# Optimization experiments

Measured on AMD Instinct MI355X. Metric: run time of the kernel, lower is better.

The kernel has to match this reference:

```python
import jax, jax.numpy as jnp
import numpy as np

B, N, M = 32, 512, 32          # batch frames, atoms, neighbors
H_A = 64                        # atom embedding dim
DMIN, DMAX, STEP = 0.0, 10.0, 0.1
FILTERS = jnp.arange(DMIN, DMAX + STEP, STEP, dtype=jnp.float32)  # [101]
H_B = FILTERS.shape[0]
N_CONV = 4
N_CLASSES = 10
BN_EPS = 1e-5


def setup_inputs() -> dict:
    key = jax.random.key(0)
    ks = jax.random.split(key, 6)
    return {
        "nbr_adj_dist": jax.random.uniform(ks[0], (B, N, M), jnp.float32) * DMAX,
        "nbr_adj_list": jax.random.randint(ks[1], (B, N, M), 0, N),
        "emb_w": jax.random.normal(ks[2], (N, H_A), jnp.float32),
        "fc_w": jax.random.normal(ks[3], (N_CONV, 2 * H_A + H_B, 2 * H_A), jnp.float32) * 0.05,
        "fc_b": jnp.zeros((N_CONV, 2 * H_A), jnp.float32),
        "bn1_g": jnp.ones((N_CONV, 2 * H_A), jnp.float32),
        "bn1_b": jnp.zeros((N_CONV, 2 * H_A), jnp.float32),
        "bn2_g": jnp.ones((N_CONV, H_A), jnp.float32),
        "bn2_b": jnp.zeros((N_CONV, H_A), jnp.float32),
        "cls_w": jax.random.normal(ks[4], (H_A, N_CLASSES), jnp.float32) * 0.05,
        "cls_b": jnp.zeros((N_CLASSES,), jnp.float32),
    }


def _bn(x2d, g, b):
    # training-mode BatchNorm1d over flattened batch axis (biased variance)
    mu = x2d.mean(axis=0)
    var = x2d.var(axis=0)
    return g * (x2d - mu) * jax.lax.rsqrt(var + BN_EPS) + b


def reference(nbr_adj_dist, nbr_adj_list, emb_w, fc_w, fc_b,
              bn1_g, bn1_b, bn2_g, bn2_b, cls_w, cls_b):
    # 1. Gaussian basis expansion of neighbor distances: [B,N,M,H_B]
    nbr_emb = jnp.exp(-((nbr_adj_dist[..., None] - FILTERS) ** 2) / (STEP ** 2))
    # 2. atom embeddings: atom_emb_idx = arange(N) per batch element
    atom = jnp.broadcast_to(emb_w[None], (B, N, H_A))
    # 3. CGCNN-style graph convolutions
    for l in range(N_CONV):
        # neighbor gather per batch: [B,N,M,H_A]
        nbrs = jax.vmap(lambda e, idx: e[idx])(atom, nbr_adj_list)
        total = jnp.concatenate(
            [jnp.broadcast_to(atom[:, :, None, :], (B, N, M, H_A)), nbrs, nbr_emb],
            axis=-1)                                        # [B,N,M,2*H_A+H_B]
        gated = jnp.einsum('bnmf,fh->bnmh', total, fc_w[l]) + fc_b[l]
        gated = _bn(gated.reshape(-1, 2 * H_A), bn1_g[l], bn1_b[l]).reshape(B, N, M, 2 * H_A)
        filt, core = jnp.split(gated, 2, axis=-1)
        summed = jnp.sum(jax.nn.sigmoid(filt) * jax.nn.relu(core), axis=2)  # [B,N,H_A]
        summed = _bn(summed.reshape(-1, H_A), bn2_g[l], bn2_b[l]).reshape(B, N, H_A)
        atom = jax.nn.relu(atom + summed)  # layer-internal residual
    # 4-6. activation, mean pooling over atoms, classifier, softmax
    emb = jax.nn.relu(atom)
    pooled = jnp.sum(emb, axis=1) / N                      # [B,H_A]
    logits = pooled @ cls_w + cls_b                        # [B,n_classes]
    return jax.nn.softmax(logits, axis=-1)
```

## Files before the change

kernel.cpp:

```cpp
#include <hip/hip_runtime.h>
#include <math.h>

constexpr int kB   = 32;
constexpr int kN   = 512;
constexpr int kM   = 32;
constexpr int kHA  = 64;
constexpr int kHB  = 101;
constexpr int kHO  = 128;
constexpr int kNF  = 229;
constexpr int kRows = kB * kN;
constexpr long kTRows = (long)kRows * kM;
constexpr int kNCls = 10;
constexpr float kEps = 1e-5f;
constexpr int kG    = 16;
constexpr int kNB   = kRows / kG;
constexpr int kT    = 512;
constexpr int kTaps = 8;

__global__ void k_init_atom(const float* __restrict__ emb, float* __restrict__ atom) {
    int i = blockIdx.x * blockDim.x + threadIdx.x;
    atom[i] = emb[i & (kN * kHA - 1)];
}

template<bool RESID>
__global__ __launch_bounds__(256)
void k_pre(const float* __restrict__ atomIn, float* __restrict__ atomOut,
           const float* __restrict__ summed, const float* __restrict__ sc2,
           const float* __restrict__ W, const float* __restrict__ bias,
           float* __restrict__ preA, float* __restrict__ preB) {
    __shared__ float sA[32 * 64];
    int t = threadIdx.x;
    int r0 = blockIdx.x * 32;
    for (int i = t; i < 32 * 64; i += 256) {
        int r = i >> 6, h = i & 63;
        float v = atomIn[(r0 + r) * 64 + h];
        if (RESID) {
            float x = fmaf(summed[(r0 + r) * 64 + h], sc2[h], sc2[64 + h]);
            v = fmaxf(v + x, 0.f);
            atomOut[(r0 + r) * 64 + h] = v;
        }
        sA[i] = v;
    }
    __syncthreads();
    int cg = t & 31, rg = t >> 5;
    const float* Wb = W + cg * 4;
    float4 accA[4], accB[4];
    float4 b4 = *(const float4*)&bias[cg * 4];
    #pragma unroll
    for (int r = 0; r < 4; ++r) {
        accA[r] = b4;
        accB[r] = make_float4(0.f, 0.f, 0.f, 0.f);
    }
    for (int k = 0; k < 64; ++k) {
        float4 wA = *(const float4*)&Wb[k * kHO];
        float4 wB = *(const float4*)&Wb[(64 + k) * kHO];
        #pragma unroll
        for (int r = 0; r < 4; ++r) {
            float a = sA[(rg * 4 + r) * 64 + k];
            accA[r].x = fmaf(a, wA.x, accA[r].x);
            accA[r].y = fmaf(a, wA.y, accA[r].y);
            accA[r].z = fmaf(a, wA.z, accA[r].z);
            accA[r].w = fmaf(a, wA.w, accA[r].w);
            accB[r].x = fmaf(a, wB.x, accB[r].x);
            accB[r].y = fmaf(a, wB.y, accB[r].y);
            accB[r].z = fmaf(a, wB.z, accB[r].z);
            accB[r].w = fmaf(a, wB.w, accB[r].w);
        }
    }
    #pragma unroll
    for (int r = 0; r < 4; ++r) {
        int row = r0 + rg * 4 + r;
        *(float4*)&preA[row * kHO + cg * 4] = accA[r];
        *(float4*)&preB[row * kHO + cg * 4] = accB[r];
    }
}

__device__ __forceinline__ void setup_tiles(int t, int blk,
        const float* __restrict__ dist, const int* __restrict__ nbrs,
        float (*wv)[kM][kTaps], int (*roff)[kM], int (*wbase)[kM]) {
    int g = t >> 5, m = t & 31;
    int p = blk * kG + g;
    float d = dist[p * kM + m];
    int kc = (int)floorf(d * 10.f);
    int ks = min(max(kc - 3, 0), kHB - kTaps);
    wbase[g][m] = ks * kHO;
    roff[g][m] = (((p >> 9) << 9) + nbrs[p * kM + m]) * kHO;
    #pragma unroll
    for (int j = 0; j < kTaps; ++j) {
        float dd = d - 0.1f * (float)(ks + j);
        wv[g][m][j] = __expf(-100.f * dd * dd);
    }
}

__device__ __forceinline__ void compute_x(const float* __restrict__ W3s,
        const float* __restrict__ wvp, int wb, int ro, int cg,
        const float* __restrict__ preB, float2 pa01, float2 pa23,
        float& x0, float& x1, float& x2, float& x3) {
    float2 xb01 = *(const float2*)&preB[ro + 2 * cg];
    float2 xb23 = *(const float2*)&preB[ro + 64 + 2 * cg];
    x0 = pa01.x + xb01.x; x1 = pa01.y + xb01.y;
    x2 = pa23.x + xb23.x; x3 = pa23.y + xb23.y;
    float warr[kTaps];
    *(float4*)&warr[0] = *(const float4*)&wvp[0];
    *(float4*)&warr[4] = *(const float4*)&wvp[4];
    const float* base = &W3s[wb + 2 * cg];
    #pragma unroll
    for (int j = 0; j < kTaps; ++j) {
        float2 a = *(const float2*)&base[j * kHO];
        float2 b = *(const float2*)&base[j * kHO + 64];
        x0 = fmaf(warr[j], a.x, x0);
        x1 = fmaf(warr[j], a.y, x1);
        x2 = fmaf(warr[j], b.x, x2);
        x3 = fmaf(warr[j], b.y, x3);
    }
}

__global__ __launch_bounds__(kT, 4)
void k_stats(const float* __restrict__ dist, const int* __restrict__ nbrs,
             const float* __restrict__ preA, const float* __restrict__ preB,
             const float* __restrict__ W3, float* __restrict__ part1) {
    __shared__ float W3s[kHB * kHO];
    __shared__ float wv[kG][kM][kTaps];
    __shared__ int   roff[kG][kM];
    __shared__ int   wbase[kG][kM];
    __shared__ float red[1024];
    int t = threadIdx.x;
    for (int i = t; i < kHB * kHO; i += kT) W3s[i] = W3[i];
    setup_tiles(t, blockIdx.x, dist, nbrs, wv, roff, wbase);
    __syncthreads();
    int cg = t & 31, ms = t >> 5;
    float S[4] = {0.f, 0.f, 0.f, 0.f}, SS[4] = {0.f, 0.f, 0.f, 0.f};
    for (int g = 0; g < kG; ++g) {
        int p = blockIdx.x * kG + g;
        float2 pa01 = *(const float2*)&preA[p * kHO + 2 * cg];
        float2 pa23 = *(const float2*)&preA[p * kHO + 64 + 2 * cg];
        #pragma unroll
        for (int mm = 0; mm < 2; ++mm) {
            int m = ms + mm * 16;
            float x0, x1, x2, x3;
            compute_x(W3s, &wv[g][m][0], wbase[g][m], roff[g][m], cg,
                      preB, pa01, pa23, x0, x1, x2, x3);
            S[0] += x0; S[1] += x1; S[2] += x2; S[3] += x3;
            SS[0] = fmaf(x0, x0, SS[0]); SS[1] = fmaf(x1, x1, SS[1]);
            SS[2] = fmaf(x2, x2, SS[2]); SS[3] = fmaf(x3, x3, SS[3]);
        }
    }
    #pragma unroll
    for (int c = 0; c < 4; ++c) {
        S[c]  += __shfl_xor(S[c], 32);
        SS[c] += __shfl_xor(SS[c], 32);
    }
    int w = t >> 6;
    if ((t & 63) < 32)
        *(float4*)&red[(w * 32 + cg) * 4] = make_float4(S[0], S[1], S[2], S[3]);
    __syncthreads();
    if (t < 128) {
        int c = t >> 5, cc = t & 31;
        float s = 0.f;
        #pragma unroll
        for (int ww = 0; ww < 8; ++ww) s += red[(ww * 32 + cc) * 4 + c];
        int ch = (c < 2) ? (2 * cc + c) : (64 + 2 * cc + (c - 2));
        part1[blockIdx.x * 256 + ch] = s;
    }
    __syncthreads();
    if ((t & 63) < 32)
        *(float4*)&red[(w * 32 + cg) * 4] = make_float4(SS[0], SS[1], SS[2], SS[3]);
    __syncthreads();
    if (t < 128) {
        int c = t >> 5, cc = t & 31;
        float s = 0.f;
        #pragma unroll
        for (int ww = 0; ww < 8; ++ww) s += red[(ww * 32 + cc) * 4 + c];
        int ch = (c < 2) ? (2 * cc + c) : (64 + 2 * cc + (c - 2));
        part1[blockIdx.x * 256 + 128 + ch] = s;
    }
}

__global__ __launch_bounds__(256)
void k_bn1r(const float* __restrict__ part1, const float* __restrict__ g,
            const float* __restrict__ bb, float* __restrict__ sc) {
    __shared__ float red[256];
    int t = threadIdx.x;
    float a0 = 0.f, a1 = 0.f, a2 = 0.f, a3 = 0.f;
    for (int r = 0; r < kNB; r += 4) {
        a0 += part1[(r + 0) * 256 + t];
        a1 += part1[(r + 1) * 256 + t];
        a2 += part1[(r + 2) * 256 + t];
        a3 += part1[(r + 3) * 256 + t];
    }
    red[t] = (a0 + a1) + (a2 + a3);
    __syncthreads();
    if (t < 128) {
        float inv = 1.f / (float)kTRows;
        float mu = red[t] * inv;
        float var = red[128 + t] * inv - mu * mu;
        float scale = g[t] * rsqrtf(var + kEps);
        sc[t] = scale;
        sc[128 + t] = bb[t] - mu * scale;
    }
}

__global__ __launch_bounds__(kT, 4)
void k_apply(const float* __restrict__ dist, const int* __restrict__ nbrs,
             const float* __restrict__ preA, const float* __restrict__ preB,
             const float* __restrict__ W3, const float* __restrict__ sc,
             float* __restrict__ summed, float* __restrict__ part2) {
    __shared__ float W3s[kHB * kHO];
    __shared__ float wv[kG][kM][kTaps];
    __shared__ int   roff[kG][kM];
    __shared__ int   wbase[kG][kM];
    __shared__ float red[1024];
    int t = threadIdx.x;
    for (int i = t; i < kHB * kHO; i += kT) W3s[i] = W3[i];
    setup_tiles(t, blockIdx.x, dist, nbrs, wv, roff, wbase);
    int cg = t & 31, ms = t >> 5;
    float scf0 = sc[2 * cg],       scf1 = sc[2 * cg + 1];
    float shf0 = sc[128 + 2 * cg], shf1 = sc[128 + 2 * cg + 1];
    float scc0 = sc[64 + 2 * cg],  scc1 = sc[64 + 2 * cg + 1];
    float shc0 = sc[192 + 2 * cg], shc1 = sc[192 + 2 * cg + 1];
    __syncthreads();
    float S2 = 0.f, SS2 = 0.f;
    for (int g = 0; g < kG; ++g) {
        int p = blockIdx.x * kG + g;
        float2 pa01 = *(const float2*)&preA[p * kHO + 2 * cg];
        float2 pa23 = *(const float2*)&preA[p * kHO + 64 + 2 * cg];
        float s0 = 0.f, s1 = 0.f;
        #pragma unroll
        for (int mm = 0; mm < 2; ++mm) {
            int m = ms + mm * 16;
            float x0, x1, x2, x3;
            compute_x(W3s, &wv[g][m][0], wbase[g][m], roff[g][m], cg,
                      preB, pa01, pa23, x0, x1, x2, x3);
            float yf0 = fmaf(x0, scf0, shf0);
            float yf1 = fmaf(x1, scf1, shf1);
            float yc0 = fmaf(x2, scc0, shc0);
            float yc1 = fmaf(x3, scc1, shc1);
            float sg0 = 1.f / (1.f + __expf(-yf0));
            float sg1 = 1.f / (1.f + __expf(-yf1));
            s0 = fmaf(sg0, fmaxf(yc0, 0.f), s0);
            s1 = fmaf(sg1, fmaxf(yc1, 0.f), s1);
        }
        *(float2*)&red[(ms * 32 + cg) * 2] = make_float2(s0, s1);
        __syncthreads();
        if (t < 64) {
            float v = 0.f;
            #pragma unroll
            for (int m2 = 0; m2 < 16; ++m2)
                v += red[(m2 * 32 + (t >> 1)) * 2 + (t & 1)];
            summed[p * kHA + t] = v;
            S2 += v;
            SS2 = fmaf(v, v, SS2);
        }
        __syncthreads();
    }
    if (t < 64) {
        part2[blockIdx.x * kHO + t] = S2;
        part2[blockIdx.x * kHO + 64 + t] = SS2;
    }
}

__global__ __launch_bounds__(128)
void k_bn2r(const float* __restrict__ part2, const float* __restrict__ g,
            const float* __restrict__ bb, float* __restrict__ sc) {
    __shared__ float red[128];
    int t = threadIdx.x;
    float a0 = 0.f, a1 = 0.f, a2 = 0.f, a3 = 0.f;
    for (int r = 0; r < kNB; r += 4) {
        a0 += part2[(r + 0) * kHO + t];
        a1 += part2[(r + 1) * kHO + t];
        a2 += part2[(r + 2) * kHO + t];
        a3 += part2[(r + 3) * kHO + t];
    }
    red[t] = (a0 + a1) + (a2 + a3);
    __syncthreads();
    if (t < 64) {
        float inv = 1.f / (float)kRows;
        float mu = red[t] * inv;
        float var = red[64 + t] * inv - mu * mu;
        float scale = g[t] * rsqrtf(var + kEps);
        sc[t] = scale;
        sc[64 + t] = bb[t] - mu * scale;
    }
}

__global__ __launch_bounds__(1024)
void k_final(const float* __restrict__ atom, const float* __restrict__ summed,
             const float* __restrict__ sc2, const float* __restrict__ cw,
             const float* __restrict__ cb, float* __restrict__ out) {
    __shared__ float red[1024];
    __shared__ float pooled[kHA];
    __shared__ float lg[kNCls];
    int b = blockIdx.x, t = threadIdx.x;
    int h = t & 63, q = t >> 6;
    const float* ab = atom + (long)b * kN * kHA;
    const float* sb = summed + (long)b * kN * kHA;
    float scv = sc2[h], shv = sc2[64 + h];
    float s = 0.f;
    for (int n = q * 32; n < q * 32 + 32; ++n) {
        float v = ab[n * 64 + h] + fmaf(sb[n * 64 + h], scv, shv);
        s += fmaxf(v, 0.f);
    }
    red[t] = s;
    __syncthreads();
    if (t < 64) {
        float v = 0.f;
        #pragma unroll
        for (int qq = 0; qq < 16; ++qq) v += red[qq * 64 + t];
        pooled[t] = v * (1.f / kN);
    }
    __syncthreads();
    if (t < kNCls) {
        float acc = cb[t];
        #pragma unroll
        for (int k = 0; k < kHA; ++k) acc = fmaf(pooled[k], cw[k * kNCls + t], acc);
        lg[t] = acc;
    }
    __syncthreads();
    if (t == 0) {
        float mx = lg[0];
        for (int c = 1; c < kNCls; ++c) mx = fmaxf(mx, lg[c]);
        float e[kNCls], se = 0.f;
        for (int c = 0; c < kNCls; ++c) { e[c] = __expf(lg[c] - mx); se += e[c]; }
        float inv = 1.f / se;
        for (int c = 0; c < kNCls; ++c) out[b * kNCls + c] = e[c] * inv;
    }
}

extern "C" void kernel_launch(void* const* d_in, const int* in_sizes, int n_in,
                              void* d_out, int out_size, void* d_ws, size_t ws_size,
                              hipStream_t stream) {
    const float* dist = (const float*)d_in[0];
    const int*   nbrs = (const int*)d_in[1];
    const float* emb  = (const float*)d_in[2];
    const float* fcw  = (const float*)d_in[3];
    const float* fcb  = (const float*)d_in[4];
    const float* bn1g = (const float*)d_in[5];
    const float* bn1b = (const float*)d_in[6];
    const float* bn2g = (const float*)d_in[7];
    const float* bn2b = (const float*)d_in[8];
    const float* clw  = (const float*)d_in[9];
    const float* clb  = (const float*)d_in[10];
    float* out = (float*)d_out;

    float* ws     = (float*)d_ws;
    float* atom   = ws;
    float* preA   = atom + kRows * kHA;
    float* preB   = preA + kRows * kHO;
    float* summed = preB + kRows * kHO;
    float* part1  = summed + kRows * kHA;
    float* part2  = part1 + kNB * 256;
    float* bn1sc  = part2 + kNB * kHO;
    float* bn2sc  = bn1sc + 256;

    k_init_atom<<<dim3(kRows * kHA / 256), dim3(256), 0, stream>>>(emb, atom);
    for (int l = 0; l < 4; ++l) {
        const float* W  = fcw + (long)l * kNF * kHO;
        const float* W3 = W + 2 * kHA * kHO;
        if (l == 0)
            k_pre<false><<<dim3(kRows / 32), dim3(256), 0, stream>>>(
                atom, atom, nullptr, nullptr, W, fcb + l * kHO, preA, preB);
        else
            k_pre<true><<<dim3(kRows / 32), dim3(256), 0, stream>>>(
                atom, atom, summed, bn2sc, W, fcb + l * kHO, preA, preB);
        k_stats<<<dim3(kNB), dim3(kT), 0, stream>>>(dist, nbrs, preA, preB, W3, part1);
        k_bn1r<<<dim3(1), dim3(256), 0, stream>>>(part1, bn1g + l * kHO, bn1b + l * kHO, bn1sc);
        k_apply<<<dim3(kNB), dim3(kT), 0, stream>>>(dist, nbrs, preA, preB, W3, bn1sc,
                                                    summed, part2);
        k_bn2r<<<dim3(1), dim3(128), 0, stream>>>(part2, bn2g + l * kHA, bn2b + l * kHA, bn2sc);
    }
    k_final<<<dim3(kB), dim3(1024), 0, stream>>>(atom, summed, bn2sc, clw, clb, out);
}
```

Before: 810.7 us.

## Fuse BN reductions via atomics, store W3 as fp16, interleave channels, halve group size

```diff
diff --git a/kernel.cpp b/kernel.cpp
--- a/kernel.cpp
+++ b/kernel.cpp
@@ -1,5 +1,8 @@
 #include <hip/hip_runtime.h>
 #include <math.h>
+
+typedef _Float16 half_t;
+typedef __attribute__((ext_vector_type(4))) _Float16 half4;
 
 constexpr int kB   = 32;
 constexpr int kN   = 512;
@@ -12,11 +15,15 @@
 constexpr long kTRows = (long)kRows * kM;
 constexpr int kNCls = 10;
 constexpr float kEps = 1e-5f;
-constexpr int kG    = 16;
+constexpr int kG    = 8;
 constexpr int kNB   = kRows / kG;
 constexpr int kT    = 512;
 constexpr int kTaps = 8;
 
+__device__ __forceinline__ int origCh(int j) {
+    return ((j & 1) << 6) + ((j >> 2) << 1) + ((j >> 1) & 1);
+}
+
 __global__ void k_init_atom(const float* __restrict__ emb, float* __restrict__ atom) {
     int i = blockIdx.x * blockDim.x + threadIdx.x;
     atom[i] = emb[i & (kN * kHA - 1)];
@@ -25,121 +32,128 @@
 template<bool RESID>
 __global__ __launch_bounds__(256)
 void k_pre(const float* __restrict__ atomIn, float* __restrict__ atomOut,
-           const float* __restrict__ summed, const float* __restrict__ sc2,
+           const float* __restrict__ summed, const float* __restrict__ acc2,
+           const float* __restrict__ g2, const float* __restrict__ b2,
            const float* __restrict__ W, const float* __restrict__ bias,
-           float* __restrict__ preA, float* __restrict__ preB) {
+           float* __restrict__ preA, float* __restrict__ preB,
+           float* __restrict__ bn1acc, float* __restrict__ zeroBuf) {
     __shared__ float sA[32 * 64];
+    __shared__ float sc2s[128];
     int t = threadIdx.x;
+    if (blockIdx.x == 0) {
+        bn1acc[t] = 0.f;
+        if (t < 128) zeroBuf[t] = 0.f;
+    }
+    if (RESID) {
+        if (t < 64) {
+            float inv = 1.f / (float)kRows;
+            float mu = acc2[t] * inv;
+            float var = acc2[64 + t] * inv - mu * mu;
+            float sc = g2[t] * rsqrtf(var + kEps);
+            sc2s[t] = sc;
+            sc2s[64 + t] = b2[t] - mu * sc;
+        }
+        __syncthreads();
+    }
     int r0 = blockIdx.x * 32;
     for (int i = t; i < 32 * 64; i += 256) {
-        int r = i >> 6, h = i & 63;
-        float v = atomIn[(r0 + r) * 64 + h];
+        float v = atomIn[r0 * 64 + i];
         if (RESID) {
-            float x = fmaf(summed[(r0 + r) * 64 + h], sc2[h], sc2[64 + h]);
-            v = fmaxf(v + x, 0.f);
-            atomOut[(r0 + r) * 64 + h] = v;
+            int h = i & 63;
+            v = fmaxf(v + fmaf(summed[r0 * 64 + i], sc2s[h], sc2s[64 + h]), 0.f);
+            atomOut[r0 * 64 + i] = v;
         }
         sA[i] = v;
     }
     __syncthreads();
     int cg = t & 31, rg = t >> 5;
-    const float* Wb = W + cg * 4;
+    float2 bb01 = *(const float2*)&bias[2 * cg];
+    float2 bb23 = *(const float2*)&bias[64 + 2 * cg];
     float4 accA[4], accB[4];
-    float4 b4 = *(const float4*)&bias[cg * 4];
     #pragma unroll
     for (int r = 0; r < 4; ++r) {
-        accA[r] = b4;
+        accA[r] = make_float4(bb01.x, bb23.x, bb01.y, bb23.y);
         accB[r] = make_float4(0.f, 0.f, 0.f, 0.f);
     }
     for (int k = 0; k < 64; ++k) {
-        float4 wA = *(const float4*)&Wb[k * kHO];
-        float4 wB = *(const float4*)&Wb[(64 + k) * kHO];
+        float2 wA01 = *(const float2*)&W[k * kHO + 2 * cg];
+        float2 wA23 = *(const float2*)&W[k * kHO + 64 + 2 * cg];
+        float2 wB01 = *(const float2*)&W[(64 + k) * kHO + 2 * cg];
+        float2 wB23 = *(const float2*)&W[(64 + k) * kHO + 64 + 2 * cg];
         #pragma unroll
         for (int r = 0; r < 4; ++r) {
             float a = sA[(rg * 4 + r) * 64 + k];
-            accA[r].x = fmaf(a, wA.x, accA[r].x);
-            accA[r].y = fmaf(a, wA.y, accA[r].y);
-            accA[r].z = fmaf(a, wA.z, accA[r].z);
-            accA[r].w = fmaf(a, wA.w, accA[r].w);
-            accB[r].x = fmaf(a, wB.x, accB[r].x);
-            accB[r].y = fmaf(a, wB.y, accB[r].y);
-            accB[r].z = fmaf(a, wB.z, accB[r].z);
-            accB[r].w = fmaf(a, wB.w, accB[r].w);
+            accA[r].x = fmaf(a, wA01.x, accA[r].x);
+            accA[r].y = fmaf(a, wA23.x, accA[r].y);
+            accA[r].z = fmaf(a, wA01.y, accA[r].z);
+            accA[r].w = fmaf(a, wA23.y, accA[r].w);
+            accB[r].x = fmaf(a, wB01.x, accB[r].x);
+            accB[r].y = fmaf(a, wB23.x, accB[r].y);
+            accB[r].z = fmaf(a, wB01.y, accB[r].z);
+            accB[r].w = fmaf(a, wB23.y, accB[r].w);
         }
     }
     #pragma unroll
     for (int r = 0; r < 4; ++r) {
         int row = r0 + rg * 4 + r;
-        *(float4*)&preA[row * kHO + cg * 4] = accA[r];
-        *(float4*)&preB[row * kHO + cg * 4] = accB[r];
-    }
-}
-
-__device__ __forceinline__ void setup_tiles(int t, int blk,
-        const float* __restrict__ dist, const int* __restrict__ nbrs,
-        float (*wv)[kM][kTaps], int (*roff)[kM], int (*wbase)[kM]) {
-    int g = t >> 5, m = t & 31;
-    int p = blk * kG + g;
-    float d = dist[p * kM + m];
-    int kc = (int)floorf(d * 10.f);
-    int ks = min(max(kc - 3, 0), kHB - kTaps);
-    wbase[g][m] = ks * kHO;
-    roff[g][m] = (((p >> 9) << 9) + nbrs[p * kM + m]) * kHO;
-    #pragma unroll
-    for (int j = 0; j < kTaps; ++j) {
-        float dd = d - 0.1f * (float)(ks + j);
-        wv[g][m][j] = __expf(-100.f * dd * dd);
-    }
-}
-
-__device__ __forceinline__ void compute_x(const float* __restrict__ W3s,
-        const float* __restrict__ wvp, int wb, int ro, int cg,
-        const float* __restrict__ preB, float2 pa01, float2 pa23,
-        float& x0, float& x1, float& x2, float& x3) {
-    float2 xb01 = *(const float2*)&preB[ro + 2 * cg];
-    float2 xb23 = *(const float2*)&preB[ro + 64 + 2 * cg];
-    x0 = pa01.x + xb01.x; x1 = pa01.y + xb01.y;
-    x2 = pa23.x + xb23.x; x3 = pa23.y + xb23.y;
-    float warr[kTaps];
-    *(float4*)&warr[0] = *(const float4*)&wvp[0];
-    *(float4*)&warr[4] = *(const float4*)&wvp[4];
-    const float* base = &W3s[wb + 2 * cg];
-    #pragma unroll
-    for (int j = 0; j < kTaps; ++j) {
-        float2 a = *(const float2*)&base[j * kHO];
-        float2 b = *(const float2*)&base[j * kHO + 64];
-        x0 = fmaf(warr[j], a.x, x0);
-        x1 = fmaf(warr[j], a.y, x1);
-        x2 = fmaf(warr[j], b.x, x2);
-        x3 = fmaf(warr[j], b.y, x3);
-    }
-}
-
-__global__ __launch_bounds__(kT, 4)
+        *(float4*)&preA[row * kHO + 4 * cg] = accA[r];
+        *(float4*)&preB[row * kHO + 4 * cg] = accB[r];
+    }
+}
+
+__global__ __launch_bounds__(kT, 6)
 void k_stats(const float* __restrict__ dist, const int* __restrict__ nbrs,
              const float* __restrict__ preA, const float* __restrict__ preB,
-             const float* __restrict__ W3, float* __restrict__ part1) {
-    __shared__ float W3s[kHB * kHO];
+             const float* __restrict__ W3, float* __restrict__ acc) {
+    __shared__ half_t W3h[kHB * kHO];
     __shared__ float wv[kG][kM][kTaps];
     __shared__ int   roff[kG][kM];
     __shared__ int   wbase[kG][kM];
-    __shared__ float red[1024];
+    __shared__ float red[2048];
     int t = threadIdx.x;
-    for (int i = t; i < kHB * kHO; i += kT) W3s[i] = W3[i];
-    setup_tiles(t, blockIdx.x, dist, nbrs, wv, roff, wbase);
+    int lb = (int)(blockIdx.x & 7) * (kNB / 8) + (int)(blockIdx.x >> 3);
+    for (int i = t; i < kHB * kHO; i += kT)
+        W3h[i] = (half_t)W3[(i & ~127) + origCh(i & 127)];
+    if (t < kG * kM) {
+        int g = t >> 5, m = t & 31;
+        int p = lb * kG + g;
+        float d = dist[p * kM + m];
+        int kc = (int)floorf(d * 10.f);
+        int ks = min(max(kc - 3, 0), kHB - kTaps);
+        wbase[g][m] = ks * kHO;
+        roff[g][m] = (((p >> 9) << 9) + nbrs[p * kM + m]) * kHO;
+        #pragma unroll
+        for (int j = 0; j < kTaps; ++j) {
+            float dd = d - 0.1f * (float)(ks + j);
+            wv[g][m][j] = __expf(-100.f * dd * dd);
+        }
+    }
     __syncthreads();
     int cg = t & 31, ms = t >> 5;
     float S[4] = {0.f, 0.f, 0.f, 0.f}, SS[4] = {0.f, 0.f, 0.f, 0.f};
     for (int g = 0; g < kG; ++g) {
-        int p = blockIdx.x * kG + g;
-        float2 pa01 = *(const float2*)&preA[p * kHO + 2 * cg];
-        float2 pa23 = *(const float2*)&preA[p * kHO + 64 + 2 * cg];
+        int p = lb * kG + g;
+        float4 pa = *(const float4*)&preA[p * kHO + 4 * cg];
         #pragma unroll
         for (int mm = 0; mm < 2; ++mm) {
             int m = ms + mm * 16;
-            float x0, x1, x2, x3;
-            compute_x(W3s, &wv[g][m][0], wbase[g][m], roff[g][m], cg,
-                      preB, pa01, pa23, x0, x1, x2, x3);
+            int ro = roff[g][m], wb = wbase[g][m];
+            float4 pb = *(const float4*)&preB[ro + 4 * cg];
+            float x0 = pa.x + pb.x, x1 = pa.y + pb.y;
+            float x2 = pa.z + pb.z, x3 = pa.w + pb.w;
+            float warr[kTaps];
+            *(float4*)&warr[0] = *(const float4*)&wv[g][m][0];
+            *(float4*)&warr[4] = *(const float4*)&wv[g][m][4];
+            const half_t* hb = &W3h[wb + 4 * cg];
+            #pragma unroll
+            for (int j = 0; j < kTaps; ++j) {
+                half4 hv = *(const half4*)&hb[j * kHO];
+                float w = warr[j];
+                x0 = fmaf(w, (float)hv.x, x0);
+                x1 = fmaf(w, (float)hv.y, x1);
+                x2 = fmaf(w, (float)hv.z, x2);
+                x3 = fmaf(w, (float)hv.w, x3);
+            }
             S[0] += x0; S[1] += x1; S[2] += x2; S[3] += x3;
             SS[0] = fmaf(x0, x0, SS[0]); SS[1] = fmaf(x1, x1, SS[1]);
             SS[2] = fmaf(x2, x2, SS[2]); SS[3] = fmaf(x3, x3, SS[3]);
@@ -151,102 +165,107 @@
         SS[c] += __shfl_xor(SS[c], 32);
     }
     int w = t >> 6;
-    if ((t & 63) < 32)
-        *(float4*)&red[(w * 32 + cg) * 4] = make_float4(S[0], S[1], S[2], S[3]);
-    __syncthreads();
-    if (t < 128) {
-        int c = t >> 5, cc = t & 31;
+    if ((t & 63) < 32) {
+        *(float4*)&red[w * 128 + cg * 4] = make_float4(S[0], S[1], S[2], S[3]);
+        *(float4*)&red[1024 + w * 128 + cg * 4] = make_float4(SS[0], SS[1], SS[2], SS[3]);
+    }
+    __syncthreads();
+    if (t < 256) {
+        int j = t & 127, sel = t >> 7;
         float s = 0.f;
         #pragma unroll
-        for (int ww = 0; ww < 8; ++ww) s += red[(ww * 32 + cc) * 4 + c];
-        int ch = (c < 2) ? (2 * cc + c) : (64 + 2 * cc + (c - 2));
-        part1[blockIdx.x * 256 + ch] = s;
-    }
-    __syncthreads();
-    if ((t & 63) < 32)
-        *(float4*)&red[(w * 32 + cg) * 4] = make_float4(SS[0], SS[1], SS[2], SS[3]);
-    __syncthreads();
-    if (t < 128) {
-        int c = t >> 5, cc = t & 31;
-        float s = 0.f;
-        #pragma unroll
-        for (int ww = 0; ww < 8; ++ww) s += red[(ww * 32 + cc) * 4 + c];
-        int ch = (c < 2) ? (2 * cc + c) : (64 + 2 * cc + (c - 2));
-        part1[blockIdx.x * 256 + 128 + ch] = s;
-    }
-}
-
-__global__ __launch_bounds__(256)
-void k_bn1r(const float* __restrict__ part1, const float* __restrict__ g,
-            const float* __restrict__ bb, float* __restrict__ sc) {
-    __shared__ float red[256];
-    int t = threadIdx.x;
-    float a0 = 0.f, a1 = 0.f, a2 = 0.f, a3 = 0.f;
-    for (int r = 0; r < kNB; r += 4) {
-        a0 += part1[(r + 0) * 256 + t];
-        a1 += part1[(r + 1) * 256 + t];
-        a2 += part1[(r + 2) * 256 + t];
-        a3 += part1[(r + 3) * 256 + t];
-    }
-    red[t] = (a0 + a1) + (a2 + a3);
-    __syncthreads();
-    if (t < 128) {
-        float inv = 1.f / (float)kTRows;
-        float mu = red[t] * inv;
-        float var = red[128 + t] * inv - mu * mu;
-        float scale = g[t] * rsqrtf(var + kEps);
-        sc[t] = scale;
-        sc[128 + t] = bb[t] - mu * scale;
-    }
-}
-
-__global__ __launch_bounds__(kT, 4)
+        for (int ww = 0; ww < 8; ++ww) s += red[sel * 1024 + ww * 128 + j];
+        atomicAdd(&acc[sel * 128 + j], s);
+    }
+}
+
+__global__ __launch_bounds__(kT, 6)
 void k_apply(const float* __restrict__ dist, const int* __restrict__ nbrs,
              const float* __restrict__ preA, const float* __restrict__ preB,
-             const float* __restrict__ W3, const float* __restrict__ sc,
-             float* __restrict__ summed, float* __restrict__ part2) {
-    __shared__ float W3s[kHB * kHO];
+             const float* __restrict__ W3, const float* __restrict__ acc,
+             const float* __restrict__ g1, const float* __restrict__ b1,
+             float* __restrict__ summed, float* __restrict__ acc2) {
+    __shared__ half_t W3h[kHB * kHO];
     __shared__ float wv[kG][kM][kTaps];
     __shared__ int   roff[kG][kM];
     __shared__ int   wbase[kG][kM];
-    __shared__ float red[1024];
+    __shared__ float red2[512];
+    __shared__ float scP[128], shP[128];
     int t = threadIdx.x;
-    for (int i = t; i < kHB * kHO; i += kT) W3s[i] = W3[i];
-    setup_tiles(t, blockIdx.x, dist, nbrs, wv, roff, wbase);
+    int lb = (int)(blockIdx.x & 7) * (kNB / 8) + (int)(blockIdx.x >> 3);
+    for (int i = t; i < kHB * kHO; i += kT)
+        W3h[i] = (half_t)W3[(i & ~127) + origCh(i & 127)];
+    if (t < kG * kM) {
+        int g = t >> 5, m = t & 31;
+        int p = lb * kG + g;
+        float d = dist[p * kM + m];
+        int kc = (int)floorf(d * 10.f);
+        int ks = min(max(kc - 3, 0), kHB - kTaps);
+        wbase[g][m] = ks * kHO;
+        roff[g][m] = (((p >> 9) << 9) + nbrs[p * kM + m]) * kHO;
+        #pragma unroll
+        for (int j = 0; j < kTaps; ++j) {
+            float dd = d - 0.1f * (float)(ks + j);
+            wv[g][m][j] = __expf(-100.f * dd * dd);
+        }
+    }
+    if (t < 128) {
+        float inv = 1.f / (float)kTRows;
+        int oc = origCh(t);
+        float mu = acc[t] * inv;
+        float var = acc[128 + t] * inv - mu * mu;
+        float sc = g1[oc] * rsqrtf(var + kEps);
+        scP[t] = sc;
+        shP[t] = b1[oc] - mu * sc;
+    }
+    __syncthreads();
     int cg = t & 31, ms = t >> 5;
-    float scf0 = sc[2 * cg],       scf1 = sc[2 * cg + 1];
-    float shf0 = sc[128 + 2 * cg], shf1 = sc[128 + 2 * cg + 1];
-    float scc0 = sc[64 + 2 * cg],  scc1 = sc[64 + 2 * cg + 1];
-    float shc0 = sc[192 + 2 * cg], shc1 = sc[192 + 2 * cg + 1];
-    __syncthreads();
+    float4 sc4 = *(const float4*)&scP[4 * cg];
+    float4 sh4 = *(const float4*)&shP[4 * cg];
     float S2 = 0.f, SS2 = 0.f;
     for (int g = 0; g < kG; ++g) {
-        int p = blockIdx.x * kG + g;
-        float2 pa01 = *(const float2*)&preA[p * kHO + 2 * cg];
-        float2 pa23 = *(const float2*)&preA[p * kHO + 64 + 2 * cg];
+        int p = lb * kG + g;
+        float4 pa = *(const float4*)&preA[p * kHO + 4 * cg];
         float s0 = 0.f, s1 = 0.f;
         #pragma unroll
         for (int mm = 0; mm < 2; ++mm) {
             int m = ms + mm * 16;
-            float x0, x1, x2, x3;
-            compute_x(W3s, &wv[g][m][0], wbase[g][m], roff[g][m], cg,
-                      preB, pa01, pa23, x0, x1, x2, x3);
-            float yf0 = fmaf(x0, scf0, shf0);
-            float yf1 = fmaf(x1, scf1, shf1);
-            float yc0 = fmaf(x2, scc0, shc0);
-            float yc1 = fmaf(x3, scc1, shc1);
+            int ro = roff[g][m], wb = wbase[g][m];
+            float4 pb = *(const float4*)&preB[ro + 4 * cg];
+            float x0 = pa.x + pb.x, x1 = pa.y + pb.y;
+            float x2 = pa.z + pb.z, x3 = pa.w + pb.w;
+            float warr[kTaps];
+            *(float4*)&warr[0] = *(const float4*)&wv[g][m][0];
+            *(float4*)&warr[4] = *(const float4*)&wv[g][m][4];
+            const half_t* hb = &W3h[wb + 4 * cg];
+            #pragma unroll
+            for (int j = 0; j < kTaps; ++j) {
+                half4 hv = *(const half4*)&hb[j * kHO];
+                float w = warr[j];
+                x0 = fmaf(w, (float)hv.x, x0);
+                x1 = fmaf(w, (float)hv.y, x1);
+                x2 = fmaf(w, (float)hv.z, x2);
+                x3 = fmaf(w, (float)hv.w, x3);
+            }
+            float yf0 = fmaf(x0, sc4.x, sh4.x);
+            float yc0 = fmaf(x1, sc4.y, sh4.y);
+            float yf1 = fmaf(x2, sc4.z, sh4.z);
+            float yc1 = fmaf(x3, sc4.w, sh4.w);
             float sg0 = 1.f / (1.f + __expf(-yf0));
             float sg1 = 1.f / (1.f + __expf(-yf1));
             s0 = fmaf(sg0, fmaxf(yc0, 0.f), s0);
             s1 = fmaf(sg1, fmaxf(yc1, 0.f), s1);
         }
-        *(float2*)&red[(ms * 32 + cg) * 2] = make_float2(s0, s1);
+        s0 += __shfl_xor(s0, 32);
+        s1 += __shfl_xor(s1, 32);
+        int w = t >> 6;
+        if ((t & 63) < 32)
+            *(float2*)&red2[w * 64 + cg * 2] = make_float2(s0, s1);
         __syncthreads();
         if (t < 64) {
             float v = 0.f;
             #pragma unroll
-            for (int m2 = 0; m2 < 16; ++m2)
-                v += red[(m2 * 32 + (t >> 1)) * 2 + (t & 1)];
+            for (int ww = 0; ww < 8; ++ww) v += red2[ww * 64 + t];
             summed[p * kHA + t] = v;
             S2 += v;
             SS2 = fmaf(v, v, SS2);
@@ -254,47 +273,34 @@
         __syncthreads();
     }
     if (t < 64) {
-        part2[blockIdx.x * kHO + t] = S2;
-        part2[blockIdx.x * kHO + 64 + t] = SS2;
-    }
-}
-
-__global__ __launch_bounds__(128)
-void k_bn2r(const float* __restrict__ part2, const float* __restrict__ g,
-            const float* __restrict__ bb, float* __restrict__ sc) {
-    __shared__ float red[128];
-    int t = threadIdx.x;
-    float a0 = 0.f, a1 = 0.f, a2 = 0.f, a3 = 0.f;
-    for (int r = 0; r < kNB; r += 4) {
-        a0 += part2[(r + 0) * kHO + t];
-        a1 += part2[(r + 1) * kHO + t];
-        a2 += part2[(r + 2) * kHO + t];
-        a3 += part2[(r + 3) * kHO + t];
-    }
-    red[t] = (a0 + a1) + (a2 + a3);
-    __syncthreads();
-    if (t < 64) {
-        float inv = 1.f / (float)kRows;
-        float mu = red[t] * inv;
-        float var = red[64 + t] * inv - mu * mu;
-        float scale = g[t] * rsqrtf(var + kEps);
-        sc[t] = scale;
-        sc[64 + t] = bb[t] - mu * scale;
+        atomicAdd(&acc2[t], S2);
+        atomicAdd(&acc2[64 + t], SS2);
     }
 }
 
 __global__ __launch_bounds__(1024)
 void k_final(const float* __restrict__ atom, const float* __restrict__ summed,
-             const float* __restrict__ sc2, const float* __restrict__ cw,
+             const float* __restrict__ acc2, const float* __restrict__ g2,
+             const float* __restrict__ b2, const float* __restrict__ cw,
              const float* __restrict__ cb, float* __restrict__ out) {
     __shared__ float red[1024];
+    __shared__ float sc2s[128];
     __shared__ float pooled[kHA];
     __shared__ float lg[kNCls];
     int b = blockIdx.x, t = threadIdx.x;
+    if (t < 64) {
+        float inv = 1.f / (float)kRows;
+        float mu = acc2[t] * inv;
+        float var = acc2[64 + t] * inv - mu * mu;
+        float sc = g2[t] * rsqrtf(var + kEps);
+        sc2s[t] = sc;
+        sc2s[64 + t] = b2[t] - mu * sc;
+    }
+    __syncthreads();
     int h = t & 63, q = t >> 6;
     const float* ab = atom + (long)b * kN * kHA;
     const float* sb = summed + (long)b * kN * kHA;
-    float scv = sc2[h], shv = sc2[64 + h];
+    float scv = sc2s[h], shv = sc2s[64 + h];
     float s = 0.f;
     for (int n = q * 32; n < q * 32 + 32; ++n) {
         float v = ab[n * 64 + h] + fmaf(sb[n * 64 + h], scv, shv);
@@ -310,10 +316,10 @@
     }
     __syncthreads();
     if (t < kNCls) {
-        float acc = cb[t];
-        #pragma unroll
-        for (int k = 0; k < kHA; ++k) acc = fmaf(pooled[k], cw[k * kNCls + t], acc);
-        lg[t] = acc;
+        float a = cb[t];
+        #pragma unroll
+        for (int k = 0; k < kHA; ++k) a = fmaf(pooled[k], cw[k * kNCls + t], a);
+        lg[t] = a;
     }
     __syncthreads();
     if (t == 0) {
@@ -347,26 +353,30 @@
     float* preA   = atom + kRows * kHA;
     float* preB   = preA + kRows * kHO;
     float* summed = preB + kRows * kHO;
-    float* part1  = summed + kRows * kHA;
-    float* part2  = part1 + kNB * 256;
-    float* bn1sc  = part2 + kNB * kHO;
-    float* bn2sc  = bn1sc + 256;
+    float* bn1acc = summed + kRows * kHA;
+    float* acc2a  = bn1acc + 256;
+    float* acc2b  = acc2a + 128;
 
     k_init_atom<<<dim3(kRows * kHA / 256), dim3(256), 0, stream>>>(emb, atom);
     for (int l = 0; l < 4; ++l) {
         const float* W  = fcw + (long)l * kNF * kHO;
         const float* W3 = W + 2 * kHA * kHO;
+        float* accW = (l & 1) ? acc2b : acc2a;
+        float* accR = ((l - 1) & 1) ? acc2b : acc2a;
         if (l == 0)
             k_pre<false><<<dim3(kRows / 32), dim3(256), 0, stream>>>(
-                atom, atom, nullptr, nullptr, W, fcb + l * kHO, preA, preB);
+                atom, atom, nullptr, nullptr, nullptr, nullptr,
+                W, fcb + l * kHO, preA, preB, bn1acc, accW);
         else
             k_pre<true><<<dim3(kRows / 32), dim3(256), 0, stream>>>(
-                atom, atom, summed, bn2sc, W, fcb + l * kHO, preA, preB);
-        k_stats<<<dim3(kNB), dim3(kT), 0, stream>>>(dist, nbrs, preA, preB, W3, part1);
-        k_bn1r<<<dim3(1), dim3(256), 0, stream>>>(part1, bn1g + l * kHO, bn1b + l * kHO, bn1sc);
-        k_apply<<<dim3(kNB), dim3(kT), 0, stream>>>(dist, nbrs, preA, preB, W3, bn1sc,
-                                                    summed, part2);
-        k_bn2r<<<dim3(1), dim3(128), 0, stream>>>(part2, bn2g + l * kHA, bn2b + l * kHA, bn2sc);
-    }
-    k_final<<<dim3(kB), dim3(1024), 0, stream>>>(atom, summed, bn2sc, clw, clb, out);
-}
+                atom, atom, summed, accR, bn2g + (l - 1) * kHA, bn2b + (l - 1) * kHA,
+                W, fcb + l * kHO, preA, preB, bn1acc, accW);
+        k_stats<<<dim3(kNB), dim3(kT), 0, stream>>>(dist, nbrs, preA, preB, W3, bn1acc);
+        k_apply<<<dim3(kNB), dim3(kT), 0, stream>>>(dist, nbrs, preA, preB, W3, bn1acc,
+                                                    bn1g + l * kHO, bn1b + l * kHO,
+                                                    summed, accW);
+    }
+    k_final<<<dim3(kB), dim3(1024), 0, stream>>>(atom, summed, acc2b,
+                                                 bn2g + 3 * kHA, bn2b + 3 * kHA,
+                                                 clw, clb, out);
+}
```

Result: faster. 744.6 us (-8.2%).
